# Optimization experiments

Hardware: AMD Instinct MI355X
Metric: run time of the kernel (lower is better)

The kernel has to match this reference:

```python
import jax, jax.numpy as jnp
import numpy as np


def setup_inputs() -> dict:
    key = jax.random.key(0)
    B, N, D = 32, 1024, 1024
    x = jax.random.normal(key, (B, N, D), dtype=jnp.float32)
    return {"x": x}


def reference(x) -> jnp.ndarray:
    # query = key = value = x (the module's Linear layers are unused).
    # kl_divs[b,i,j] = KL(softmax(x[b,i]) || softmax(x[b,j])) for i != j, 0 on diag.
    # Since KL(p||p) == 0, the full vectorized KL matrix matches the looped version.
    logp = jax.nn.log_softmax(x, axis=-1)          # [B, N, D]
    p = jnp.exp(logp)                               # softmax(x)
    neg_ent = jnp.sum(p * logp, axis=-1)            # [B, N]  = sum p log p
    cross = jnp.einsum('bid,bjd->bij', p, logp)     # [B, N, N] = sum_d p_i log q_j
    kl = neg_ent[:, :, None] - cross                # [B, N, N]
    attn = jax.nn.softmax(-kl, axis=-1)             # [B, N, N]
    out = jnp.einsum('bij,bjd->bid', attn, x)       # value = x
    return out
```

## Files before the change

### kernel.cpp

```cpp
#include <hip/hip_runtime.h>
#include <hip/hip_bf16.h>
#include <stdint.h>

#define B_ 32
#define N_ 1024
#define D_ 1024

typedef __bf16 bf16x8 __attribute__((ext_vector_type(8)));
typedef float f32x4 __attribute__((ext_vector_type(4)));

static __device__ __forceinline__ unsigned short f2bf(float f) {
    union { float f; unsigned u; } v; v.f = f;
    unsigned r = v.u + 0x7fffu + ((v.u >> 16) & 1u);
    return (unsigned short)(r >> 16);
}

static __device__ __forceinline__ void gld_lds16(const void* g, void* l) {
    __builtin_amdgcn_global_load_lds(
        (const __attribute__((address_space(1))) void*)g,
        (__attribute__((address_space(3))) void*)l, 16, 0, 0);
}

__global__ __launch_bounds__(256) void prep_kernel(const float* __restrict__ x,
        unsigned short* __restrict__ pb, unsigned short* __restrict__ xb,
        float* __restrict__ lse) {
    int row = blockIdx.x;
    const float4* xr = (const float4*)(x + (size_t)row * D_);
    int t = threadIdx.x;
    float4 v = xr[t];

    float m = fmaxf(fmaxf(v.x, v.y), fmaxf(v.z, v.w));
    for (int o = 32; o > 0; o >>= 1) m = fmaxf(m, __shfl_xor(m, o, 64));
    __shared__ float redm[4];
    __shared__ float reds[4];
    int wave = t >> 6, lane = t & 63;
    if (lane == 0) redm[wave] = m;
    __syncthreads();
    m = fmaxf(fmaxf(redm[0], redm[1]), fmaxf(redm[2], redm[3]));

    float e0 = expf(v.x - m), e1 = expf(v.y - m);
    float e2 = expf(v.z - m), e3 = expf(v.w - m);
    float s = e0 + e1 + e2 + e3;
    for (int o = 32; o > 0; o >>= 1) s += __shfl_xor(s, o, 64);
    if (lane == 0) reds[wave] = s;
    __syncthreads();
    s = reds[0] + reds[1] + reds[2] + reds[3];
    float inv = 1.0f / s;

    ushort4 pu, xu;
    pu.x = f2bf(e0 * inv); pu.y = f2bf(e1 * inv);
    pu.z = f2bf(e2 * inv); pu.w = f2bf(e3 * inv);
    xu.x = f2bf(v.x); xu.y = f2bf(v.y); xu.z = f2bf(v.z); xu.w = f2bf(v.w);
    ((ushort4*)(pb + (size_t)row * D_))[t] = pu;
    ((ushort4*)(xb + (size_t)row * D_))[t] = xu;
    if (t == 0) lse[row] = m + logf(s);
}

__global__ __launch_bounds__(256) void gemm_bt(const unsigned short* __restrict__ Ag,
        const unsigned short* __restrict__ Bg, float* __restrict__ Cg,
        const float* __restrict__ bias) {
    const int K = 1024;
    int b = blockIdx.z;
    const unsigned short* A  = Ag + (size_t)b * N_ * K;
    const unsigned short* Bm = Bg + (size_t)b * N_ * K;
    float* C = Cg + (size_t)b * (size_t)N_ * N_;
    int m0 = blockIdx.y * 128, n0 = blockIdx.x * 128;

    __shared__ unsigned short lds[2][128 * 32];
    int t = threadIdx.x;
    int wave = t >> 6, lane = t & 63;
    int wr = wave >> 1, wc = wave & 1;

    f32x4 acc[4][4];
    #pragma unroll
    for (int i = 0; i < 4; i++)
        #pragma unroll
        for (int j = 0; j < 4; j++)
            #pragma unroll
            for (int r = 0; r < 4; r++) acc[i][j][r] = 0.0f;

    int fm = lane & 15;
    int fk = (lane >> 4) * 8;

    for (int k0 = 0; k0 < K; k0 += 32) {
        __syncthreads();
        #pragma unroll
        for (int h = 0; h < 2; h++) {
            int c = h * 256 + t;
            int r = c >> 2, col = (c & 3) * 8;
            gld_lds16(A  + (size_t)(m0 + r) * K + k0 + col, (char*)&lds[0][0] + c * 16);
            gld_lds16(Bm + (size_t)(n0 + r) * K + k0 + col, (char*)&lds[1][0] + c * 16);
        }
        __syncthreads();

        bf16x8 av[4], bv[4];
        #pragma unroll
        for (int i = 0; i < 4; i++) {
            av[i] = *(const bf16x8*)&lds[0][(wr * 64 + i * 16 + fm) * 32 + fk];
            bv[i] = *(const bf16x8*)&lds[1][(wc * 64 + i * 16 + fm) * 32 + fk];
        }
        #pragma unroll
        for (int i = 0; i < 4; i++)
            #pragma unroll
            for (int j = 0; j < 4; j++)
                acc[i][j] = __builtin_amdgcn_mfma_f32_16x16x32_bf16(av[i], bv[j], acc[i][j], 0, 0, 0);
    }

    int cr = (lane >> 4) * 4;
    int cc = lane & 15;
    #pragma unroll
    for (int i = 0; i < 4; i++) {
        int row = m0 + wr * 64 + i * 16 + cr;
        #pragma unroll
        for (int j = 0; j < 4; j++) {
            int col = n0 + wc * 64 + j * 16 + cc;
            float bvv = bias ? bias[b * N_ + col] : 0.0f;
            #pragma unroll
            for (int r = 0; r < 4; r++)
                C[(size_t)(row + r) * N_ + col] = acc[i][j][r] - bvv;
        }
    }
}

__global__ __launch_bounds__(256) void softmax_kernel(const float* __restrict__ S,
        unsigned short* __restrict__ attn) {
    size_t row = blockIdx.x;
    const float4* sr = (const float4*)(S + row * N_);
    int t = threadIdx.x;
    float4 v = sr[t];

    float m = fmaxf(fmaxf(v.x, v.y), fmaxf(v.z, v.w));
    for (int o = 32; o > 0; o >>= 1) m = fmaxf(m, __shfl_xor(m, o, 64));
    __shared__ float redm[4];
    __shared__ float reds[4];
    int wave = t >> 6, lane = t & 63;
    if (lane == 0) redm[wave] = m;
    __syncthreads();
    m = fmaxf(fmaxf(redm[0], redm[1]), fmaxf(redm[2], redm[3]));

    float e0 = expf(v.x - m), e1 = expf(v.y - m);
    float e2 = expf(v.z - m), e3 = expf(v.w - m);
    float s = e0 + e1 + e2 + e3;
    for (int o = 32; o > 0; o >>= 1) s += __shfl_xor(s, o, 64);
    if (lane == 0) reds[wave] = s;
    __syncthreads();
    s = reds[0] + reds[1] + reds[2] + reds[3];
    float inv = 1.0f / s;

    ushort4 o4;
    o4.x = f2bf(e0 * inv); o4.y = f2bf(e1 * inv);
    o4.z = f2bf(e2 * inv); o4.w = f2bf(e3 * inv);
    ((ushort4*)(attn + row * N_))[t] = o4;
}

__global__ __launch_bounds__(256) void transpose_kernel(const unsigned short* __restrict__ in,
        unsigned short* __restrict__ out) {
    int b  = blockIdx.z;
    int j0 = blockIdx.y * 64;
    int d0 = blockIdx.x * 64;
    __shared__ unsigned short tile[64][72];
    const unsigned short* ip = in + ((size_t)b * N_ + j0) * D_ + d0;
    int t = threadIdx.x;
    #pragma unroll
    for (int c = t; c < 512; c += 256) {
        int r = c >> 3, col = (c & 7) * 8;
        uint4 val = *(const uint4*)(ip + (size_t)r * D_ + col);
        *(uint4*)&tile[r][col] = val;
    }
    __syncthreads();
    unsigned short* op = out + ((size_t)b * D_ + d0) * N_ + j0;
    #pragma unroll
    for (int c = t; c < 512; c += 256) {
        int r = c >> 3, col = (c & 7) * 8;
        unsigned short vals[8];
        #pragma unroll
        for (int k = 0; k < 8; k++) vals[k] = tile[col + k][r];
        uint4 o;
        o.x = (unsigned)vals[0] | ((unsigned)vals[1] << 16);
        o.y = (unsigned)vals[2] | ((unsigned)vals[3] << 16);
        o.z = (unsigned)vals[4] | ((unsigned)vals[5] << 16);
        o.w = (unsigned)vals[6] | ((unsigned)vals[7] << 16);
        *(uint4*)(op + (size_t)r * N_ + col) = o;
    }
}

extern "C" void kernel_launch(void* const* d_in, const int* in_sizes, int n_in,
                              void* d_out, int out_size, void* d_ws, size_t ws_size,
                              hipStream_t stream) {
    const float* x = (const float*)d_in[0];
    float* out = (float*)d_out;
    char* ws = (char*)d_ws;

    unsigned short* pb   = (unsigned short*)(ws);
    unsigned short* xb   = (unsigned short*)(ws + 67108864ULL);
    float*          lse  = (float*)(ws + 134217728ULL);
    float*          Sraw = (float*)(ws + 135266304ULL);
    unsigned short* xbT  = (unsigned short*)Sraw;
    unsigned short* attn = pb;

    prep_kernel<<<dim3(B_ * N_), 256, 0, stream>>>(x, pb, xb, lse);
    gemm_bt<<<dim3(8, 8, B_), 256, 0, stream>>>(pb, xb, Sraw, lse);
    softmax_kernel<<<dim3(B_ * N_), 256, 0, stream>>>(Sraw, attn);
    transpose_kernel<<<dim3(16, 16, B_), 256, 0, stream>>>(xb, xbT);
    gemm_bt<<<dim3(8, 8, B_), 256, 0, stream>>>(attn, xbT, out, nullptr);
}
```

Measured before the change: 507.4 us.

## Fuse softmax into GEMM epilogues with lse-shifted exponent and deferred normalization

Removes the separate softmax pass over the fp32 score matrix. The first GEMM's epilogue computes exp(cross - lse_j), stores it as bf16 and accumulates row sums with atomics. The second GEMM divides by the row sum in its epilogue. The change also XOR-swizzles the GEMM LDS layout to avoid bank conflicts, gives the prep kernel one row per wave with no block syncs, and pads the transpose tile differently. It relies on exp(-KL) never overflowing, which holds because the shifted exponent is bounded by neg_ent, and it adds atomic traffic plus a memset.

```diff
diff --git a/kernel.cpp b/kernel.cpp
--- a/kernel.cpp
+++ b/kernel.cpp
@@ -24,46 +24,56 @@
 __global__ __launch_bounds__(256) void prep_kernel(const float* __restrict__ x,
         unsigned short* __restrict__ pb, unsigned short* __restrict__ xb,
         float* __restrict__ lse) {
-    int row = blockIdx.x;
+    int row  = blockIdx.x * 4 + (threadIdx.x >> 6);
+    int lane = threadIdx.x & 63;
     const float4* xr = (const float4*)(x + (size_t)row * D_);
-    int t = threadIdx.x;
-    float4 v = xr[t];
-
-    float m = fmaxf(fmaxf(v.x, v.y), fmaxf(v.z, v.w));
-    for (int o = 32; o > 0; o >>= 1) m = fmaxf(m, __shfl_xor(m, o, 64));
-    __shared__ float redm[4];
-    __shared__ float reds[4];
-    int wave = t >> 6, lane = t & 63;
-    if (lane == 0) redm[wave] = m;
-    __syncthreads();
-    m = fmaxf(fmaxf(redm[0], redm[1]), fmaxf(redm[2], redm[3]));
-
-    float e0 = expf(v.x - m), e1 = expf(v.y - m);
-    float e2 = expf(v.z - m), e3 = expf(v.w - m);
-    float s = e0 + e1 + e2 + e3;
-    for (int o = 32; o > 0; o >>= 1) s += __shfl_xor(s, o, 64);
-    if (lane == 0) reds[wave] = s;
-    __syncthreads();
-    s = reds[0] + reds[1] + reds[2] + reds[3];
+
+    float4 v[4];
+    #pragma unroll
+    for (int q = 0; q < 4; q++) v[q] = xr[lane + 64 * q];
+
+    float m = -1e30f;
+    #pragma unroll
+    for (int q = 0; q < 4; q++)
+        m = fmaxf(m, fmaxf(fmaxf(v[q].x, v[q].y), fmaxf(v[q].z, v[q].w)));
+    #pragma unroll
+    for (int o = 1; o < 64; o <<= 1) m = fmaxf(m, __shfl_xor(m, o, 64));
+
+    float4 e[4];
+    float s = 0.0f;
+    #pragma unroll
+    for (int q = 0; q < 4; q++) {
+        e[q].x = __expf(v[q].x - m); e[q].y = __expf(v[q].y - m);
+        e[q].z = __expf(v[q].z - m); e[q].w = __expf(v[q].w - m);
+        s += e[q].x + e[q].y + e[q].z + e[q].w;
+    }
+    #pragma unroll
+    for (int o = 1; o < 64; o <<= 1) s += __shfl_xor(s, o, 64);
     float inv = 1.0f / s;
 
-    ushort4 pu, xu;
-    pu.x = f2bf(e0 * inv); pu.y = f2bf(e1 * inv);
-    pu.z = f2bf(e2 * inv); pu.w = f2bf(e3 * inv);
-    xu.x = f2bf(v.x); xu.y = f2bf(v.y); xu.z = f2bf(v.z); xu.w = f2bf(v.w);
-    ((ushort4*)(pb + (size_t)row * D_))[t] = pu;
-    ((ushort4*)(xb + (size_t)row * D_))[t] = xu;
-    if (t == 0) lse[row] = m + logf(s);
-}
-
+    ushort4* pr = (ushort4*)(pb + (size_t)row * D_);
+    ushort4* xw = (ushort4*)(xb + (size_t)row * D_);
+    #pragma unroll
+    for (int q = 0; q < 4; q++) {
+        ushort4 pu, xu;
+        pu.x = f2bf(e[q].x * inv); pu.y = f2bf(e[q].y * inv);
+        pu.z = f2bf(e[q].z * inv); pu.w = f2bf(e[q].w * inv);
+        xu.x = f2bf(v[q].x); xu.y = f2bf(v[q].y);
+        xu.z = f2bf(v[q].z); xu.w = f2bf(v[q].w);
+        pr[lane + 64 * q] = pu;
+        xw[lane + 64 * q] = xu;
+    }
+    if (lane == 0) lse[row] = m + logf(s);
+}
+
+template<int MODE>
 __global__ __launch_bounds__(256) void gemm_bt(const unsigned short* __restrict__ Ag,
-        const unsigned short* __restrict__ Bg, float* __restrict__ Cg,
-        const float* __restrict__ bias) {
+        const unsigned short* __restrict__ Bg, void* __restrict__ Cg,
+        const float* __restrict__ lse, float* __restrict__ rowsum) {
     const int K = 1024;
     int b = blockIdx.z;
     const unsigned short* A  = Ag + (size_t)b * N_ * K;
     const unsigned short* Bm = Bg + (size_t)b * N_ * K;
-    float* C = Cg + (size_t)b * (size_t)N_ * N_;
     int m0 = blockIdx.y * 128, n0 = blockIdx.x * 128;
 
     __shared__ unsigned short lds[2][128 * 32];
@@ -80,24 +90,27 @@
             for (int r = 0; r < 4; r++) acc[i][j][r] = 0.0f;
 
     int fm = lane & 15;
-    int fk = (lane >> 4) * 8;
+    int gf = lane >> 4;
 
     for (int k0 = 0; k0 < K; k0 += 32) {
         __syncthreads();
         #pragma unroll
         for (int h = 0; h < 2; h++) {
             int c = h * 256 + t;
-            int r = c >> 2, col = (c & 3) * 8;
-            gld_lds16(A  + (size_t)(m0 + r) * K + k0 + col, (char*)&lds[0][0] + c * 16);
-            gld_lds16(Bm + (size_t)(n0 + r) * K + k0 + col, (char*)&lds[1][0] + c * 16);
+            int r = c >> 2;
+            int g = (c & 3) ^ ((r >> 1) & 3);
+            gld_lds16(A  + (size_t)(m0 + r) * K + k0 + g * 8, (char*)&lds[0][0] + c * 16);
+            gld_lds16(Bm + (size_t)(n0 + r) * K + k0 + g * 8, (char*)&lds[1][0] + c * 16);
         }
         __syncthreads();
 
         bf16x8 av[4], bv[4];
         #pragma unroll
         for (int i = 0; i < 4; i++) {
-            av[i] = *(const bf16x8*)&lds[0][(wr * 64 + i * 16 + fm) * 32 + fk];
-            bv[i] = *(const bf16x8*)&lds[1][(wc * 64 + i * 16 + fm) * 32 + fk];
+            int ra = wr * 64 + i * 16 + fm;
+            int rb = wc * 64 + i * 16 + fm;
+            av[i] = *(const bf16x8*)&lds[0][ra * 32 + ((gf ^ ((ra >> 1) & 3)) * 8)];
+            bv[i] = *(const bf16x8*)&lds[1][rb * 32 + ((gf ^ ((rb >> 1) & 3)) * 8)];
         }
         #pragma unroll
         for (int i = 0; i < 4; i++)
@@ -108,49 +121,65 @@
 
     int cr = (lane >> 4) * 4;
     int cc = lane & 15;
-    #pragma unroll
-    for (int i = 0; i < 4; i++) {
-        int row = m0 + wr * 64 + i * 16 + cr;
-        #pragma unroll
-        for (int j = 0; j < 4; j++) {
-            int col = n0 + wc * 64 + j * 16 + cc;
-            float bvv = bias ? bias[b * N_ + col] : 0.0f;
-            #pragma unroll
-            for (int r = 0; r < 4; r++)
-                C[(size_t)(row + r) * N_ + col] = acc[i][j][r] - bvv;
-        }
-    }
-}
-
-__global__ __launch_bounds__(256) void softmax_kernel(const float* __restrict__ S,
-        unsigned short* __restrict__ attn) {
-    size_t row = blockIdx.x;
-    const float4* sr = (const float4*)(S + row * N_);
-    int t = threadIdx.x;
-    float4 v = sr[t];
-
-    float m = fmaxf(fmaxf(v.x, v.y), fmaxf(v.z, v.w));
-    for (int o = 32; o > 0; o >>= 1) m = fmaxf(m, __shfl_xor(m, o, 64));
-    __shared__ float redm[4];
-    __shared__ float reds[4];
-    int wave = t >> 6, lane = t & 63;
-    if (lane == 0) redm[wave] = m;
-    __syncthreads();
-    m = fmaxf(fmaxf(redm[0], redm[1]), fmaxf(redm[2], redm[3]));
-
-    float e0 = expf(v.x - m), e1 = expf(v.y - m);
-    float e2 = expf(v.z - m), e3 = expf(v.w - m);
-    float s = e0 + e1 + e2 + e3;
-    for (int o = 32; o > 0; o >>= 1) s += __shfl_xor(s, o, 64);
-    if (lane == 0) reds[wave] = s;
-    __syncthreads();
-    s = reds[0] + reds[1] + reds[2] + reds[3];
-    float inv = 1.0f / s;
-
-    ushort4 o4;
-    o4.x = f2bf(e0 * inv); o4.y = f2bf(e1 * inv);
-    o4.z = f2bf(e2 * inv); o4.w = f2bf(e3 * inv);
-    ((ushort4*)(attn + row * N_))[t] = o4;
+
+    if (MODE == 0) {
+        unsigned short* Co = (unsigned short*)Cg + (size_t)b * (size_t)N_ * N_;
+        float lsev[4];
+        #pragma unroll
+        for (int j = 0; j < 4; j++) lsev[j] = lse[b * N_ + n0 + wc * 64 + j * 16 + cc];
+        float rsum[16];
+        #pragma unroll
+        for (int q = 0; q < 16; q++) rsum[q] = 0.0f;
+        #pragma unroll
+        for (int i = 0; i < 4; i++) {
+            #pragma unroll
+            for (int r = 0; r < 4; r++) {
+                int row = m0 + wr * 64 + i * 16 + cr + r;
+                size_t ro = (size_t)row * N_;
+                #pragma unroll
+                for (int j = 0; j < 4; j++) {
+                    int col = n0 + wc * 64 + j * 16 + cc;
+                    float ev = __expf(acc[i][j][r] - lsev[j]);
+                    unsigned short eb = f2bf(ev);
+                    union { unsigned u; float f; } bk; bk.u = ((unsigned)eb) << 16;
+                    Co[ro + col] = eb;
+                    rsum[i * 4 + r] += bk.f;
+                }
+            }
+        }
+        #pragma unroll
+        for (int q = 0; q < 16; q++) {
+            float sv = rsum[q];
+            sv += __shfl_xor(sv, 1, 64);
+            sv += __shfl_xor(sv, 2, 64);
+            sv += __shfl_xor(sv, 4, 64);
+            sv += __shfl_xor(sv, 8, 64);
+            rsum[q] = sv;
+        }
+        if (cc == 0) {
+            #pragma unroll
+            for (int q = 0; q < 16; q++) {
+                int row = m0 + wr * 64 + (q >> 2) * 16 + cr + (q & 3);
+                atomicAdd(&rowsum[b * N_ + row], rsum[q]);
+            }
+        }
+    } else {
+        float* Co = (float*)Cg + (size_t)b * (size_t)N_ * N_;
+        #pragma unroll
+        for (int i = 0; i < 4; i++) {
+            #pragma unroll
+            for (int r = 0; r < 4; r++) {
+                int row = m0 + wr * 64 + i * 16 + cr + r;
+                float inv = 1.0f / rowsum[b * N_ + row];
+                size_t ro = (size_t)row * N_;
+                #pragma unroll
+                for (int j = 0; j < 4; j++) {
+                    int col = n0 + wc * 64 + j * 16 + cc;
+                    Co[ro + col] = acc[i][j][r] * inv;
+                }
+            }
+        }
+    }
 }
 
 __global__ __launch_bounds__(256) void transpose_kernel(const unsigned short* __restrict__ in,
@@ -158,14 +187,15 @@
     int b  = blockIdx.z;
     int j0 = blockIdx.y * 64;
     int d0 = blockIdx.x * 64;
-    __shared__ unsigned short tile[64][72];
+    __shared__ unsigned short tile[64][66];
     const unsigned short* ip = in + ((size_t)b * N_ + j0) * D_ + d0;
     int t = threadIdx.x;
     #pragma unroll
     for (int c = t; c < 512; c += 256) {
         int r = c >> 3, col = (c & 7) * 8;
         uint4 val = *(const uint4*)(ip + (size_t)r * D_ + col);
-        *(uint4*)&tile[r][col] = val;
+        unsigned int* dst = (unsigned int*)&tile[r][col];
+        dst[0] = val.x; dst[1] = val.y; dst[2] = val.z; dst[3] = val.w;
     }
     __syncthreads();
     unsigned short* op = out + ((size_t)b * D_ + d0) * N_ + j0;
@@ -191,16 +221,16 @@
     float* out = (float*)d_out;
     char* ws = (char*)d_ws;
 
-    unsigned short* pb   = (unsigned short*)(ws);
-    unsigned short* xb   = (unsigned short*)(ws + 67108864ULL);
-    float*          lse  = (float*)(ws + 134217728ULL);
-    float*          Sraw = (float*)(ws + 135266304ULL);
-    unsigned short* xbT  = (unsigned short*)Sraw;
-    unsigned short* attn = pb;
-
-    prep_kernel<<<dim3(B_ * N_), 256, 0, stream>>>(x, pb, xb, lse);
-    gemm_bt<<<dim3(8, 8, B_), 256, 0, stream>>>(pb, xb, Sraw, lse);
-    softmax_kernel<<<dim3(B_ * N_), 256, 0, stream>>>(Sraw, attn);
+    unsigned short* pb    = (unsigned short*)(ws);
+    unsigned short* xb    = (unsigned short*)(ws + 67108864ULL);
+    unsigned short* xbT   = (unsigned short*)(ws + 134217728ULL);
+    unsigned short* attnE = (unsigned short*)(ws + 201326592ULL);
+    float*          lse   = (float*)(ws + 268435456ULL);
+    float*          rowsum= (float*)(ws + 268566528ULL);
+
+    hipMemsetAsync(rowsum, 0, B_ * N_ * sizeof(float), stream);
+    prep_kernel<<<dim3(B_ * N_ / 4), 256, 0, stream>>>(x, pb, xb, lse);
     transpose_kernel<<<dim3(16, 16, B_), 256, 0, stream>>>(xb, xbT);
-    gemm_bt<<<dim3(8, 8, B_), 256, 0, stream>>>(attn, xbT, out, nullptr);
-}
+    gemm_bt<0><<<dim3(8, 8, B_), 256, 0, stream>>>(pb, xb, attnE, lse, rowsum);
+    gemm_bt<1><<<dim3(8, 8, B_), 256, 0, stream>>>(attnE, xbT, out, nullptr, rowsum);
+}
```

After: 480.9 us. 5.2% less time.
